# Optimization experiments

Measured on AMD Instinct MI355X. Metric: run time of the kernel, lower is better.

## Reference

```python
import jax, jax.numpy as jnp
import numpy as np

N = 100000   # total nodes (batched molecular graph)
E = 200000   # total edges
G = 5000     # number of graphs
NF = 16      # num_node_features
EF = 8       # num_edge_features
LD = 64      # latent_dim
EPS = 1e-5   # batch-norm eps (PyG BatchNorm default)


def setup_inputs() -> dict:
    key = jax.random.key(0)
    ks = jax.random.split(key, 20)
    s = 0.1  # weight scale
    return {
        'x': jax.random.normal(ks[0], (N, NF), dtype=jnp.float32),
        'edge_index': jax.random.randint(ks[1], (2, E), 0, N, dtype=jnp.int32),
        'edge_attr': jax.random.normal(ks[2], (E, EF), dtype=jnp.float32),
        'batch': jnp.sort(jax.random.randint(ks[3], (N,), 0, G, dtype=jnp.int32)),
        # ECC layer 1 (in=16 -> out=32)
        'We1': jax.random.normal(ks[4], (NF * 32, EF), dtype=jnp.float32) * s,
        'b1': jnp.zeros((32,), dtype=jnp.float32),
        'Wr1': jax.random.normal(ks[5], (32, NF), dtype=jnp.float32) * s,
        'g1': jnp.ones((32,), dtype=jnp.float32),
        'be1': jnp.zeros((32,), dtype=jnp.float32),
        # ECC layer 2 (in=32 -> out=64)
        'We2': jax.random.normal(ks[6], (32 * 64, EF), dtype=jnp.float32) * s,
        'b2': jnp.zeros((64,), dtype=jnp.float32),
        'Wr2': jax.random.normal(ks[7], (64, 32), dtype=jnp.float32) * s,
        'g2': jnp.ones((64,), dtype=jnp.float32),
        'be2': jnp.zeros((64,), dtype=jnp.float32),
        # dense tail
        'Wf1': jax.random.normal(ks[8], (128, 64), dtype=jnp.float32) * s,
        'bf1': jnp.zeros((128,), dtype=jnp.float32),
        'Wf2': jax.random.normal(ks[9], (2 * LD, 128), dtype=jnp.float32) * s,
        'bf2': jnp.zeros((2 * LD,), dtype=jnp.float32),
    }


def _ecc(x, src, dst, edge_attr, We, b, Wr, out_c):
    # theta: per-edge [out_c, in_c] filter matrices from edge features
    in_c = x.shape[1]
    theta = (edge_attr @ We.T).reshape(-1, out_c, in_c)       # [E, out, in]
    deg = jnp.zeros((x.shape[0],), x.dtype).at[src].add(1.0)   # degree over edge_index[0]
    norm = jnp.where(deg > 0, 1.0 / deg, 0.0)                  # [N]
    msg = jnp.einsum('eoi,ei->eo', theta, x[src]) * norm[src, None]  # [E, out]
    agg = jnp.zeros((x.shape[0], out_c), x.dtype).at[dst].add(msg)   # scatter-add
    return agg + b + x @ Wr.T


def _bn(x, g, be):
    # training-mode batch norm over the node dimension
    mu = jnp.mean(x, axis=0)
    var = jnp.mean((x - mu) ** 2, axis=0)
    return (x - mu) * jax.lax.rsqrt(var + EPS) * g + be


def reference(x, edge_index, edge_attr, batch,
              We1, b1, Wr1, g1, be1,
              We2, b2, Wr2, g2, be2,
              Wf1, bf1, Wf2, bf2):
    src, dst = edge_index[0], edge_index[1]
    h = _ecc(x, src, dst, edge_attr, We1, b1, Wr1, 32)
    h = jax.nn.relu(_bn(h, g1, be1))
    h = _ecc(h, src, dst, edge_attr, We2, b2, Wr2, 64)
    h = jax.nn.relu(_bn(h, g2, be2))
    # global mean pool over graphs
    sums = jax.ops.segment_sum(h, batch, num_segments=G)
    cnts = jax.ops.segment_sum(jnp.ones((h.shape[0],), h.dtype), batch, num_segments=G)
    pooled = sums / jnp.maximum(cnts, 1.0)[:, None]            # [G, 64]
    h = jax.nn.relu(pooled @ Wf1.T + bf1)
    out = h @ Wf2.T + bf2                                      # [G, 2*LD]
    mu_z = out[:, :LD]
    log_sigma = out[:, LD:]
    return mu_z, log_sigma
```

## Files before the change

### kernel.cpp

```cpp
#include <hip/hip_runtime.h>

#define NN 100000
#define NE 200000
#define NG 5000
#define EPSI 1e-5f
#define NBLK 98

using short8 = __attribute__((ext_vector_type(8))) short;
using f32x4  = __attribute__((ext_vector_type(4))) float;

static __device__ inline short bfbits(float f) {
    __bf16 b = (__bf16)f;
    return __builtin_bit_cast(short, b);
}
static __device__ inline float bf2f(short s) {
    unsigned u = ((unsigned)(unsigned short)s) << 16;
    return __builtin_bit_cast(float, u);
}

constexpr long FZ_NRM  = 0;
constexpr long FZ_STAT = NN;
constexpr long FZ_DCNT = NN + 512;
constexpr long ZN_FAST = 2L * NN + 512;
constexpr long O_OFFS  = ZN_FAST;
constexpr long O_CURS  = O_OFFS + NN;
constexpr long O_PERM  = O_CURS + NN;
constexpr long O_GLO   = O_PERM + NE;
constexpr long O_BSUM  = O_GLO + NG + 1;
constexpr long O_POOL  = O_BSUM + 256;
constexpr long O_H1    = O_POOL + 64L * NG;
constexpr long O_OUT2  = O_H1 + 32L * NN;
constexpr long O_MSG2  = O_OUT2 + 64L * NN;
constexpr long TOTAL_FAST = O_MSG2 + 64L * NE;

constexpr long B_NORM = 0;
constexpr long B_AGG1 = NN;
constexpr long B_AGG2 = B_AGG1 + 32L * NN;
constexpr long B_GSUM = B_AGG2 + 64L * NN;
constexpr long B_GCNT = B_GSUM + 64L * NG;
constexpr long B_STAT = B_GCNT + NG;
constexpr long ZERO_FB = B_STAT + 512;


__global__ void k_norm(float* __restrict__ deg) {
    int n = blockIdx.x * blockDim.x + threadIdx.x;
    if (n < NN) { float d = deg[n]; deg[n] = d > 0.f ? 1.f / d : 0.f; }
}

template <int CI, int COLS, bool BNIN>
__global__ void __launch_bounds__(64 * (COLS / 16))
k_edge_lds(const int* __restrict__ ei, const float* __restrict__ ea,
           const float* __restrict__ h, const float* __restrict__ W,
           const float* __restrict__ nrm,
           const float* __restrict__ scin, const float* __restrict__ shin,
           float* __restrict__ msg)
{
    constexpr int KS = CI / 4;
    constexpr int TILES = COLS / 16;
    constexpr int BT = 64 * TILES;
    constexpr int HP = (CI == 32) ? 36 : 20;
    constexpr int NGRP = NE / 16;
    constexpr int TPR = BT / 16;

    const int tid  = threadIdx.x;
    const int lane = tid & 63;
    const int wid  = tid >> 6;
    const int c = lane & 15;
    const int q = lane >> 4;

    short8 bfr[KS];
    {
        const float* wrow = W + (wid * 16 + c) * (CI * 8) + q * 8;
        #pragma unroll
        for (int kk = 0; kk < KS; ++kk) {
            const float* p = wrow + kk * 32;
            #pragma unroll
            for (int j = 0; j < 8; ++j) bfr[kk][j] = bfbits(p[j]);
        }
    }

    __shared__ float h_lds[2][16 * HP];
    __shared__ float ea_lds[2][16 * 9];

    const int hrow = tid / TPR;
    const int hj0  = (tid % TPR) * 2;
    const int erow = tid >> 3;
    const int ef   = tid & 7;
    const bool eact = (tid < 128);

    float bsc0 = 1.f, bsc1 = 1.f, bsh0 = 0.f, bsh1 = 0.f;
    if constexpr (BNIN) {
        bsc0 = scin[hj0]; bsc1 = scin[hj0 + 1];
        bsh0 = shin[hj0]; bsh1 = shin[hj0 + 1];
    }

    auto write = [&](int buf, float v0, float v1, float ev) {
        if constexpr (BNIN) {
            v0 = fmaxf(fmaf(v0, bsc0, bsh0), 0.f);
            v1 = fmaxf(fmaf(v1, bsc1, bsh1), 0.f);
        }
        h_lds[buf][hrow * HP + hj0]     = v0;
        h_lds[buf][hrow * HP + hj0 + 1] = v1;
        if (eact) ea_lds[buf][erow * 9 + ef] = ev;
    };

    auto compute = [&](int buf, long e0) {
        float ev[8];
        #pragma unroll
        for (int j = 0; j < 8; ++j) ev[j] = ea_lds[buf][c * 9 + j];
        f32x4 acc = {0.f, 0.f, 0.f, 0.f};
        #pragma unroll
        for (int kk = 0; kk < KS; ++kk) {
            float hv = h_lds[buf][c * HP + kk * 4 + q];
            short8 afr;
            #pragma unroll
            for (int j = 0; j < 8; ++j) afr[j] = bfbits(hv * ev[j]);
            acc = __builtin_amdgcn_mfma_f32_16x16x32_bf16(afr, bfr[kk], acc, 0, 0, 0);
        }
        #pragma unroll
        for (int t = 0; t < 4; ++t) {
            msg[(e0 + q * 4 + t) * COLS + wid * 16 + c] = acc[t];
        }
    };

    const int GD = gridDim.x;
    int g = blockIdx.x;
    if (g >= NGRP) return;

    int sh_c = ei[(long)g * 16 + hrow];
    int se_c = 0; if (eact) se_c = ei[(long)g * 16 + erow];
    int sh_n = 0, se_n = 0;
    {
        int gn0 = g + GD;
        if (gn0 < NGRP) {
            sh_n = ei[(long)gn0 * 16 + hrow];
            if (eact) se_n = ei[(long)gn0 * 16 + erow];
        }
    }
    float hv0, hv1, eav = 0.f;
    {
        const float* hp = h + (long)sh_c * CI + hj0;
        hv0 = hp[0]; hv1 = hp[1];
        if (eact) eav = ea[((long)g * 16 + erow) * 8 + ef] * nrm[se_c];
    }
    write(0, hv0, hv1, eav);
    __syncthreads();

    int p = 0;
    for (;;) {
        int gn = g + GD;
        bool more = (gn < NGRP);
        int gnn = gn + GD;
        int sh_f = 0, se_f = 0;
        if (gnn < NGRP) {
            sh_f = ei[(long)gnn * 16 + hrow];
            if (eact) se_f = ei[(long)gnn * 16 + erow];
        }
        if (more) {
            const float* hp = h + (long)sh_n * CI + hj0;
            hv0 = hp[0]; hv1 = hp[1];
            if (eact) eav = ea[((long)gn * 16 + erow) * 8 + ef] * nrm[se_n];
        }
        compute(p, (long)g * 16);
        if (!more) break;
        write(p ^ 1, hv0, hv1, eav);
        __syncthreads();
        sh_n = sh_f; se_n = se_f;
        g = gn; p ^= 1;
    }
}

template <int KS, int COLS>
__global__ void __launch_bounds__(256) k_edge_mfma_at(
    const int* __restrict__ ei, const float* __restrict__ ea,
    const float* __restrict__ h, const float* __restrict__ W,
    const float* __restrict__ nrm, float* __restrict__ outp)
{
    constexpr int TILES = COLS / 16;
    constexpr int CI = KS * 4;
    const int lane = threadIdx.x & 63;
    const int wid  = threadIdx.x >> 6;
    const int c = lane & 15;
    const int q = lane >> 4;
    const int gw = blockIdx.x * 4 + wid;
    const int ntile = gw % TILES;
    const int grp   = gw / TILES;
    if (grp >= NE / 16) return;
    short8 bfr[KS];
    {
        const float* wrow = W + (ntile * 16 + c) * (KS * 32) + q * 8;
        #pragma unroll
        for (int kk = 0; kk < KS; ++kk) {
            const float* p = wrow + kk * 32;
            #pragma unroll
            for (int j = 0; j < 8; ++j) bfr[kk][j] = bfbits(p[j]);
        }
    }
    const long e0 = (long)grp * 16;
    const long e  = e0 + c;
    const int  s  = ei[e];
    const float nv = nrm[s];
    float ev[8];
    {
        const float* p = ea + e * 8;
        #pragma unroll
        for (int j = 0; j < 8; ++j) ev[j] = p[j];
    }
    float hv[KS];
    {
        const float* hp = h + (long)s * CI + q;
        #pragma unroll
        for (int kk = 0; kk < KS; ++kk) hv[kk] = hp[kk * 4] * nv;
    }
    f32x4 acc = {0.f, 0.f, 0.f, 0.f};
    #pragma unroll
    for (int kk = 0; kk < KS; ++kk) {
        short8 afr;
        #pragma unroll
        for (int j = 0; j < 8; ++j) afr[j] = bfbits(hv[kk] * ev[j]);
        acc = __builtin_amdgcn_mfma_f32_16x16x32_bf16(afr, bfr[kk], acc, 0, 0, 0);
    }
    #pragma unroll
    for (int t = 0; t < 4; ++t) {
        int m = q * 4 + t;
        int d = ei[NE + e0 + m];
        atomicAdd(&outp[(long)d * COLS + ntile * 16 + c], acc[t]);
    }
}

template <int C>
__global__ void k_colstats(const float* __restrict__ v, float* __restrict__ sum,
                           float* __restrict__ ssq) {
    constexpr int RPB = 256 / C;
    const int c = threadIdx.x % C;
    const int r = threadIdx.x / C;
    float s = 0.f, q = 0.f;
    for (int n = blockIdx.x * RPB + r; n < NN; n += gridDim.x * RPB) {
        float val = v[(long)n * C + c];
        s += val; q += val * val;
    }
    __shared__ float ls[256], lq[256];
    ls[threadIdx.x] = s; lq[threadIdx.x] = q;
    __syncthreads();
    if (threadIdx.x < C) {
        float ts = 0.f, tq = 0.f;
        #pragma unroll
        for (int k = 0; k < RPB; ++k) { ts += ls[c + k * C]; tq += lq[c + k * C]; }
        atomicAdd(&sum[c], ts);
        atomicAdd(&ssq[c], tq);
    }
}

__global__ void k_fin(int C, const float* __restrict__ sum, const float* __restrict__ ssq,
                      const float* __restrict__ g, const float* __restrict__ be,
                      float* __restrict__ scale, float* __restrict__ shift) {
    int c = threadIdx.x;
    if (c < C) {
        float mu  = sum[c] / (float)NN;
        float var = ssq[c] / (float)NN - mu * mu;
        float rs  = rsqrtf(var + EPSI);
        float sc  = rs * g[c];
        scale[c] = sc;
        shift[c] = be[c] - mu * sc;
    }
}

__global__ void k_bnrelu32(const float* __restrict__ in, const float* __restrict__ scale,
                           const float* __restrict__ shift, float* __restrict__ outp) {
    long t = (long)blockIdx.x * blockDim.x + threadIdx.x;
    if (t < 32L * NN) {
        int c = (int)(t & 31);
        float v = in[t] * scale[c] + shift[c];
        outp[t] = v > 0.f ? v : 0.f;
    }
}

template <int CO>
__global__ void __launch_bounds__(256) k_msum(
    const float* __restrict__ msg, const int* __restrict__ offs,
    const int* __restrict__ dcnt, const int* __restrict__ perm,
    float* __restrict__ aggout)
{
    constexpr int CPN = CO / 4;
    long t = (long)blockIdx.x * 256 + threadIdx.x;
    long n = t / CPN;
    int chunk = (int)(t % CPN);
    if (n >= NN) return;
    int lo = offs[n], ct = dcnt[n];
    f32x4 a = {0.f, 0.f, 0.f, 0.f}, b = {0.f, 0.f, 0.f, 0.f};
    int j = 0;
    for (; j + 1 < ct; j += 2) {
        int ea0 = perm[lo + j];
        int ea1 = perm[lo + j + 1];
        a += *reinterpret_cast<const f32x4*>(msg + (long)ea0 * CO + chunk * 4);
        b += *reinterpret_cast<const f32x4*>(msg + (long)ea1 * CO + chunk * 4);
    }
    if (j < ct) {
        int ea0 = perm[lo + j];
        a += *reinterpret_cast<const f32x4*>(msg + (long)ea0 * CO + chunk * 4);
    }
    a += b;
    *reinterpret_cast<f32x4*>(aggout + n * CO + chunk * 4) = a;
}

template <int CI, int CO, bool BNIN>
__global__ void __launch_bounds__(256) k_root(
    const float* __restrict__ X, const float* __restrict__ W,
    const float* __restrict__ bias, const float* __restrict__ scin,
    const float* __restrict__ shin, float* __restrict__ Y,
    float* __restrict__ sum, float* __restrict__ ssq)
{
    constexpr int TILES = CO / 16;
    constexpr int MT = NN / 16;
    constexpr int MTPB = 4 / TILES;
    const int lane = threadIdx.x & 63;
    const int wid  = threadIdx.x >> 6;
    const int c = lane & 15;
    const int q = lane >> 4;
    const int ntile = (TILES == 4) ? wid : (wid & (TILES - 1));
    const int mtoff = (TILES == 4) ? 0 : (wid >> 1);
    const int o = ntile * 16 + c;
    const bool kvalid = (q * 8) < CI;

    short8 bhi = {0,0,0,0,0,0,0,0}, blo = {0,0,0,0,0,0,0,0};
    if (kvalid) {
        const float* wrow = W + (long)o * CI + q * 8;
        #pragma unroll
        for (int j = 0; j < 8; ++j) {
            float v = wrow[j];
            short h = bfbits(v);
            bhi[j] = h;
            blo[j] = bfbits(v - bf2f(h));
        }
    }
    float bsc[8], bsh[8];
    if constexpr (BNIN) {
        #pragma unroll
        for (int j = 0; j < 8; ++j) {
            bsc[j] = kvalid ? scin[q * 8 + j] : 0.f;
            bsh[j] = kvalid ? shin[q * 8 + j] : 0.f;
        }
    }
    const float bv = bias[o];
    float s_acc = 0.f, q_acc = 0.f;

    for (int mt = blockIdx.x * MTPB + mtoff; mt < MT; mt += gridDim.x * MTPB) {
        short8 ahi = {0,0,0,0,0,0,0,0}, alo = {0,0,0,0,0,0,0,0};
        if (kvalid) {
            const float* xp = X + (long)(mt * 16 + c) * CI + q * 8;
            #pragma unroll
            for (int j = 0; j < 8; ++j) {
                float v = xp[j];
                if constexpr (BNIN) v = fmaxf(fmaf(v, bsc[j], bsh[j]), 0.f);
                short h = bfbits(v);
                ahi[j] = h;
                alo[j] = bfbits(v - bf2f(h));
            }
        }
        f32x4 acc = {0.f, 0.f, 0.f, 0.f};
        acc = __builtin_amdgcn_mfma_f32_16x16x32_bf16(ahi, bhi, acc, 0, 0, 0);
        acc = __builtin_amdgcn_mfma_f32_16x16x32_bf16(ahi, blo, acc, 0, 0, 0);
        acc = __builtin_amdgcn_mfma_f32_16x16x32_bf16(alo, bhi, acc, 0, 0, 0);
        #pragma unroll
        for (int t4 = 0; t4 < 4; ++t4) {
            long r = (long)mt * 16 + q * 4 + t4;
            long idx = r * CO + o;
            float v = Y[idx] + acc[t4] + bv;
            Y[idx] = v;
            s_acc += v;
            q_acc = fmaf(v, v, q_acc);
        }
    }

    __shared__ float ls[256], lq[256];
    ls[threadIdx.x] = s_acc; lq[threadIdx.x] = q_acc;
    __syncthreads();
    if (threadIdx.x < CO) {
        int ch = threadIdx.x;
        int bw = ch >> 4;
        int cc = ch & 15;
        float ts = 0.f, tq = 0.f;
        if (TILES == 4) {
            #pragma unroll
            for (int q2 = 0; q2 < 4; ++q2) {
                ts += ls[bw * 64 + q2 * 16 + cc];
                tq += lq[bw * 64 + q2 * 16 + cc];
            }
        } else {
            #pragma unroll
            for (int w2 = 0; w2 < 2; ++w2) {
                int w = bw + w2 * 2;
                #pragma unroll
                for (int q2 = 0; q2 < 4; ++q2) {
                    ts += ls[w * 64 + q2 * 16 + cc];
                    tq += lq[w * 64 + q2 * 16 + cc];
                }
            }
        }
        atomicAdd(&sum[ch], ts);
        atomicAdd(&ssq[ch], tq);
    }
}

template <int K, int NO, bool RELU, bool SPLITOUT>
__global__ void __launch_bounds__(256) k_fcmm(
    const float* __restrict__ X, const float* __restrict__ W,
    const float* __restrict__ bias, float* __restrict__ Y)
{
    constexpr int KS = K / 32;
    constexpr int TILES = NO / 16;
    constexpr int MT = (NG + 15) / 16;
    const int lane = threadIdx.x & 63;
    const int wid  = threadIdx.x >> 6;
    const int c = lane & 15;
    const int q = lane >> 4;
    const int gw = blockIdx.x * 4 + wid;
    const int ntile = gw % TILES;
    const int mt    = gw / TILES;
    if (mt >= MT) return;

    short8 bhi[KS], blo[KS];
    {
        const float* wrow = W + (ntile * 16 + c) * K + q * 8;
        #pragma unroll
        for (int kk = 0; kk < KS; ++kk) {
            const float* p = wrow + kk * 32;
            #pragma unroll
            for (int j = 0; j < 8; ++j) {
                float v = p[j];
                short h = bfbits(v);
                bhi[kk][j] = h;
                blo[kk][j] = bfbits(v - bf2f(h));
            }
        }
    }

    int arow = mt * 16 + c;
    if (arow > NG - 1) arow = NG - 1;
    const float* xp = X + (long)arow * K + q * 8;

    f32x4 acc = {0.f, 0.f, 0.f, 0.f};
    #pragma unroll
    for (int kk = 0; kk < KS; ++kk) {
        const float* p = xp + kk * 32;
        short8 ahi, alo;
        #pragma unroll
        for (int j = 0; j < 8; ++j) {
            float v = p[j];
            short h = bfbits(v);
            ahi[j] = h;
            alo[j] = bfbits(v - bf2f(h));
        }
        acc = __builtin_amdgcn_mfma_f32_16x16x32_bf16(ahi, bhi[kk], acc, 0, 0, 0);
        acc = __builtin_amdgcn_mfma_f32_16x16x32_bf16(ahi, blo[kk], acc, 0, 0, 0);
        acc = __builtin_amdgcn_mfma_f32_16x16x32_bf16(alo, bhi[kk], acc, 0, 0, 0);
    }

    const int o = ntile * 16 + c;
    const float bv = bias[o];
    #pragma unroll
    for (int t = 0; t < 4; ++t) {
        int r = mt * 16 + q * 4 + t;
        if (r < NG) {
            float v = acc[t] + bv;
            if (RELU) v = v > 0.f ? v : 0.f;
            if (SPLITOUT) {
                if (o < 64) Y[(long)r * 64 + o] = v;
                else        Y[(long)NG * 64 + (long)r * 64 + (o - 64)] = v;
            } else {
                Y[(long)r * NO + o] = v;
            }
        }
    }
}

__global__ void k_fc(const float* __restrict__ pooled,
                     const float* __restrict__ Wf1, const float* __restrict__ bf1,
                     const float* __restrict__ Wf2, const float* __restrict__ bf2,
                     float* __restrict__ outp) {
    const int lane = threadIdx.x & 63;
    int gw = (blockIdx.x * blockDim.x + threadIdx.x) >> 6;
    int nw = (gridDim.x * blockDim.x) >> 6;
    for (int g = gw; g < NG; g += nw) {
        float pl = pooled[(long)g * 64 + lane];
        float f1a = bf1[lane], f1b = bf1[lane + 64];
        const float* w1a = Wf1 + lane * 64;
        const float* w1b = Wf1 + (lane + 64) * 64;
        #pragma unroll 8
        for (int i = 0; i < 64; ++i) {
            float pv = __shfl(pl, i);
            f1a += pv * w1a[i];
            f1b += pv * w1b[i];
        }
        f1a = f1a > 0.f ? f1a : 0.f;
        f1b = f1b > 0.f ? f1b : 0.f;
        float oa = bf2[lane], ob = bf2[lane + 64];
        const float* w2a = Wf2 + lane * 128;
        const float* w2b = Wf2 + (lane + 64) * 128;
        #pragma unroll 8
        for (int i = 0; i < 64; ++i) {
            float va = __shfl(f1a, i);
            float vb = __shfl(f1b, i);
            oa += va * w2a[i] + vb * w2a[64 + i];
            ob += va * w2b[i] + vb * w2b[64 + i];
        }
        outp[(long)g * 64 + lane] = oa;
        outp[(long)NG * 64 + (long)g * 64 + lane] = ob;
    }
}


__global__ void k_degcnt(const int* __restrict__ ei, float* __restrict__ deg,
                         int* __restrict__ dcnt) {
    int e = blockIdx.x * blockDim.x + threadIdx.x;
    if (e < NE) {
        atomicAdd(&deg[ei[e]], 1.0f);
        atomicAdd(&dcnt[ei[NE + e]], 1);
    }
}

__global__ void k_scanA(const int* __restrict__ dcnt, int* __restrict__ offs,
                        int* __restrict__ bsum, float* __restrict__ deg) {
    int tid = threadIdx.x, b = blockIdx.x;
    int base = b * 1024 + tid * 4;
    int v[4]; int t = 0;
    #pragma unroll
    for (int k = 0; k < 4; ++k) { v[k] = (base + k < NN) ? dcnt[base + k] : 0; t += v[k]; }
    #pragma unroll
    for (int k = 0; k < 4; ++k) {
        int i = base + k;
        if (i < NN) { float d = deg[i]; deg[i] = d > 0.f ? 1.f / d : 0.f; }
    }
    __shared__ int s[256];
    s[tid] = t;
    __syncthreads();
    for (int d = 1; d < 256; d <<= 1) {
        int x = (tid >= d) ? s[tid - d] : 0;
        __syncthreads();
        s[tid] += x;
        __syncthreads();
    }
    int excl = s[tid] - t;
    int o = excl;
    #pragma unroll
    for (int k = 0; k < 4; ++k) {
        if (base + k < NN) offs[base + k] = o;
        o += v[k];
    }
    if (tid == 255) bsum[b] = s[255];
}

__global__ void k_scanB(int* __restrict__ bsum) {
    int tid = threadIdx.x;
    __shared__ int s[128];
    int val = (tid < NBLK) ? bsum[tid] : 0;
    s[tid] = val;
    __syncthreads();
    for (int d = 1; d < 128; d <<= 1) {
        int x = (tid >= d) ? s[tid - d] : 0;
        __syncthreads();
        s[tid] += x;
        __syncthreads();
    }
    bsum[tid] = s[tid] - val;
}

__global__ void k_scanC(int* __restrict__ offs, int* __restrict__ curs,
                        const int* __restrict__ bsum) {
    int tid = threadIdx.x, b = blockIdx.x;
    int base = b * 1024 + tid * 4;
    int add = bsum[b];
    #pragma unroll
    for (int k = 0; k < 4; ++k) {
        int i = base + k;
        if (i < NN) { int o = offs[i] + add; offs[i] = o; curs[i] = o; }
    }
}

__global__ void k_scatter(const int* __restrict__ ei, int* __restrict__ curs,
                          int* __restrict__ perm, const int* __restrict__ batch,
                          int* __restrict__ glo) {
    int e = blockIdx.x * blockDim.x + threadIdx.x;
    if (e < NE) {
        int d = ei[NE + e];
        int pos = atomicAdd(&curs[d], 1);
        perm[pos] = e;
    }
    if (e <= NG) {
        int lo = 0, hi = NN;
        while (lo < hi) { int m = (lo + hi) >> 1; if (batch[m] < e) lo = m + 1; else hi = m; }
        glo[e] = lo;
    }
}

__global__ void k_poolg(const float* __restrict__ out2, const int* __restrict__ glo,
                        const float* __restrict__ scale, const float* __restrict__ shift,
                        float* __restrict__ pooled) {
    const int lane = threadIdx.x & 63;
    int g = (blockIdx.x * blockDim.x + threadIdx.x) >> 6;
    if (g >= NG) return;
    int lo = glo[g], hi = glo[g + 1];
    float sc = scale[lane], sh = shift[lane];
    float acc = 0.f;
    for (int n = lo; n < hi; ++n) {
        float v = out2[(long)n * 64 + lane] * sc + sh;
        acc += v > 0.f ? v : 0.f;
    }
    float m = (float)(hi - lo);
    pooled[(long)g * 64 + lane] = acc / (m > 1.f ? m : 1.f);
}


__global__ void k_deg(const int* __restrict__ ei, float* __restrict__ deg) {
    int e = blockIdx.x * blockDim.x + threadIdx.x;
    if (e < NE) atomicAdd(&deg[ei[e]], 1.0f);
}

template <int CI, int CO>
__global__ void k_nodeadd(const float* __restrict__ xin, const float* __restrict__ Wr,
                          const float* __restrict__ b, float* __restrict__ outp) {
    constexpr int NPW = 64 / CO;
    const int lane = threadIdx.x & 63;
    const int c = lane % CO;
    const int sub = lane / CO;
    float w[CI];
    #pragma unroll
    for (int i = 0; i < CI; ++i) w[i] = Wr[c * CI + i];
    float bias = b[c];
    int gw = (blockIdx.x * blockDim.x + threadIdx.x) >> 6;
    int nw = (gridDim.x * blockDim.x) >> 6;
    for (int n0 = gw * NPW; n0 < NN; n0 += nw * NPW) {
        int n = n0 + sub;
        if (n < NN) {
            const float* xp = xin + (long)n * CI;
            float acc = outp[(long)n * CO + c] + bias;
            #pragma unroll
            for (int i = 0; i < CI; ++i) acc += xp[i] * w[i];
            outp[(long)n * CO + c] = acc;
        }
    }
}

__global__ void k_pool_at(const float* __restrict__ out2, const int* __restrict__ batch,
                          const float* __restrict__ scale, const float* __restrict__ shift,
                          float* __restrict__ gsum) {
    long t = (long)blockIdx.x * blockDim.x + threadIdx.x;
    int c = (int)(t & 63);
    long n0 = (t >> 6) * 4;
    if (n0 >= NN) return;
    float sc = scale[c], sh = shift[c];
    float acc = 0.f;
    int gprev = batch[n0];
    #pragma unroll
    for (int k = 0; k < 4; ++k) {
        long n = n0 + k;
        if (n >= NN) break;
        int g = batch[n];
        float v = out2[n * 64 + c] * sc + sh;
        v = v > 0.f ? v : 0.f;
        if (g != gprev) {
            atomicAdd(&gsum[(long)gprev * 64 + c], acc);
            acc = 0.f; gprev = g;
        }
        acc += v;
    }
    atomicAdd(&gsum[(long)gprev * 64 + c], acc);
}

__global__ void k_cnt(const int* __restrict__ batch, float* __restrict__ gcnt) {
    int n = blockIdx.x * blockDim.x + threadIdx.x;
    if (n < NN) atomicAdd(&gcnt[batch[n]], 1.0f);
}

__global__ void k_div(float* __restrict__ gsum, const float* __restrict__ gcnt) {
    long t = (long)blockIdx.x * blockDim.x + threadIdx.x;
    if (t < 64L * NG) {
        float cnt = gcnt[t >> 6];
        gsum[t] = gsum[t] / (cnt > 1.f ? cnt : 1.f);
    }
}


extern "C" void kernel_launch(void* const* d_in, const int* in_sizes, int n_in,
                              void* d_out, int out_size, void* d_ws, size_t ws_size,
                              hipStream_t stream) {
    const float* x   = (const float*)d_in[0];
    const int*   ei  = (const int*)d_in[1];
    const float* ea  = (const float*)d_in[2];
    const int*   bat = (const int*)d_in[3];
    const float* We1 = (const float*)d_in[4];
    const float* b1  = (const float*)d_in[5];
    const float* Wr1 = (const float*)d_in[6];
    const float* g1  = (const float*)d_in[7];
    const float* be1 = (const float*)d_in[8];
    const float* We2 = (const float*)d_in[9];
    const float* b2  = (const float*)d_in[10];
    const float* Wr2 = (const float*)d_in[11];
    const float* g2  = (const float*)d_in[12];
    const float* be2 = (const float*)d_in[13];
    const float* Wf1 = (const float*)d_in[14];
    const float* bf1 = (const float*)d_in[15];
    const float* Wf2 = (const float*)d_in[16];
    const float* bf2 = (const float*)d_in[17];
    float* out = (float*)d_out;
    float* ws  = (float*)d_ws;
    int*   wsi = (int*)d_ws;

    if (ws_size >= (size_t)TOTAL_FAST * sizeof(float)) {
        float* nrm    = ws + FZ_NRM;
        float* st     = ws + FZ_STAT;
        int*   dcnt   = wsi + FZ_DCNT;
        int*   offs   = wsi + O_OFFS;
        int*   curs   = wsi + O_CURS;
        int*   perm   = wsi + O_PERM;
        int*   glo    = wsi + O_GLO;
        int*   bsum   = wsi + O_BSUM;
        float* pooled = ws + O_POOL;
        float* h1     = ws + O_H1;
        float* out2   = ws + O_OUT2;
        float* msg1   = ws + O_OUT2;
        float* msg2   = ws + O_MSG2;
        float* fc1out = ws + O_MSG2;
        float* sums1 = st;        float* ssq1 = st + 32;
        float* sums2 = st + 64;   float* ssq2 = st + 128;
        float* sc1   = st + 192;  float* sh1  = st + 224;
        float* sc2   = st + 256;  float* sh2  = st + 320;

        hipMemsetAsync(d_ws, 0, (size_t)ZN_FAST * sizeof(float), stream);

        k_degcnt<<<(NE + 255) / 256, 256, 0, stream>>>(ei, nrm, dcnt);
        k_scanA<<<NBLK, 256, 0, stream>>>(dcnt, offs, bsum, nrm);
        k_scanB<<<1, 128, 0, stream>>>(bsum);
        k_scanC<<<NBLK, 256, 0, stream>>>(offs, curs, bsum);
        k_scatter<<<(NE + 255) / 256, 256, 0, stream>>>(ei, curs, perm, bat, glo);

        k_edge_lds<16, 32, false><<<2048, 128, 0, stream>>>(
            ei, ea, x, We1, nrm, nullptr, nullptr, msg1);
        k_msum<32><<<3125, 256, 0, stream>>>(msg1, offs, dcnt, perm, h1);
        k_root<16, 32, false><<<512, 256, 0, stream>>>(
            x, Wr1, b1, nullptr, nullptr, h1, sums1, ssq1);
        k_fin<<<1, 64, 0, stream>>>(32, sums1, ssq1, g1, be1, sc1, sh1);

        k_edge_lds<32, 64, true><<<2048, 256, 0, stream>>>(
            ei, ea, h1, We2, nrm, sc1, sh1, msg2);
        k_msum<64><<<6250, 256, 0, stream>>>(msg2, offs, dcnt, perm, out2);
        k_root<32, 64, true><<<512, 256, 0, stream>>>(
            h1, Wr2, b2, sc1, sh1, out2, sums2, ssq2);
        k_fin<<<1, 64, 0, stream>>>(64, sums2, ssq2, g2, be2, sc2, sh2);

        k_poolg<<<1250, 256, 0, stream>>>(out2, glo, sc2, sh2, pooled);

        {
            constexpr int MT = (NG + 15) / 16;
            k_fcmm<64, 128, true,  false><<<(MT * 8 + 3) / 4, 256, 0, stream>>>(pooled, Wf1, bf1, fc1out);
            k_fcmm<128, 128, false, true><<<(MT * 8 + 3) / 4, 256, 0, stream>>>(fc1out, Wf2, bf2, out);
        }
    } else {
        float* nrm   = ws + B_NORM;
        float* agg1  = ws + B_AGG1;
        float* agg2  = ws + B_AGG2;
        float* gsum  = ws + B_GSUM;
        float* gcnt  = ws + B_GCNT;
        float* st    = ws + B_STAT;
        float* sums1 = st;        float* ssq1 = st + 32;
        float* sums2 = st + 64;   float* ssq2 = st + 128;
        float* sc1   = st + 192;  float* sh1  = st + 224;
        float* sc2   = st + 256;  float* sh2  = st + 320;

        hipMemsetAsync(d_ws, 0, (size_t)ZERO_FB * sizeof(float), stream);

        k_deg<<<(NE + 255) / 256, 256, 0, stream>>>(ei, nrm);
        k_norm<<<(NN + 255) / 256, 256, 0, stream>>>(nrm);

        k_edge_mfma_at<4, 32><<<6250, 256, 0, stream>>>(ei, ea, x, We1, nrm, agg1);
        k_nodeadd<16, 32><<<1024, 256, 0, stream>>>(x, Wr1, b1, agg1);
        k_colstats<32><<<1024, 256, 0, stream>>>(agg1, sums1, ssq1);
        k_fin<<<1, 64, 0, stream>>>(32, sums1, ssq1, g1, be1, sc1, sh1);
        k_bnrelu32<<<(int)((32L * NN + 255) / 256), 256, 0, stream>>>(agg1, sc1, sh1, agg1);

        k_edge_mfma_at<8, 64><<<12500, 256, 0, stream>>>(ei, ea, agg1, We2, nrm, agg2);
        k_nodeadd<32, 64><<<1024, 256, 0, stream>>>(agg1, Wr2, b2, agg2);
        k_colstats<64><<<1024, 256, 0, stream>>>(agg2, sums2, ssq2);
        k_fin<<<1, 64, 0, stream>>>(64, sums2, ssq2, g2, be2, sc2, sh2);

        k_pool_at<<<6250, 256, 0, stream>>>(agg2, bat, sc2, sh2, gsum);
        k_cnt<<<(NN + 255) / 256, 256, 0, stream>>>(bat, gcnt);
        k_div<<<(int)((64L * NG + 255) / 256), 256, 0, stream>>>(gsum, gcnt);
        k_fc<<<1250, 256, 0, stream>>>(gsum, Wf1, bf1, Wf2, bf2, out);
    }
}
```

Baseline: 200.9 us.

## Store edge messages in bf16 and process 32 edges per block iteration

Per-edge messages are now written as bf16 instead of fp32, which halves the traffic of the message write and of the gather in the segment-sum kernel; k_msum converts back to fp32 before accumulating. The LDS-staged edge kernel now handles 32 edges per group using float4 loads of node features, so all threads take part in loading edge attributes. It also pads the pool offset to a 4-aligned boundary. The cost is extra rounding error in the messages and more LDS and register use per block.

After: 191.7 us. -4.6%, faster.

```diff
diff --git a/kernel.cpp b/kernel.cpp
--- a/kernel.cpp
+++ b/kernel.cpp
@@ -27,7 +27,7 @@
 constexpr long O_PERM  = O_CURS + NN;
 constexpr long O_GLO   = O_PERM + NE;
 constexpr long O_BSUM  = O_GLO + NG + 1;
-constexpr long O_POOL  = O_BSUM + 256;
+constexpr long O_POOL  = ((O_BSUM + 256 + 3) & ~3L);
 constexpr long O_H1    = O_POOL + 64L * NG;
 constexpr long O_OUT2  = O_H1 + 32L * NN;
 constexpr long O_MSG2  = O_OUT2 + 64L * NN;
@@ -53,14 +53,15 @@
            const float* __restrict__ h, const float* __restrict__ W,
            const float* __restrict__ nrm,
            const float* __restrict__ scin, const float* __restrict__ shin,
-           float* __restrict__ msg)
+           unsigned short* __restrict__ msg)
 {
     constexpr int KS = CI / 4;
     constexpr int TILES = COLS / 16;
     constexpr int BT = 64 * TILES;
     constexpr int HP = (CI == 32) ? 36 : 20;
-    constexpr int NGRP = NE / 16;
-    constexpr int TPR = BT / 16;
+    constexpr int NGRP = NE / 32;
+    constexpr int TPR = BT / 32;
+    constexpr int EPT = 256 / BT;
 
     const int tid  = threadIdx.x;
     const int lane = tid & 63;
@@ -79,47 +80,56 @@
         }
     }
 
-    __shared__ float h_lds[2][16 * HP];
-    __shared__ float ea_lds[2][16 * 9];
+    __shared__ __align__(16) float h_lds[2][32 * HP];
+    __shared__ float ea_lds[2][32 * 9];
 
     const int hrow = tid / TPR;
-    const int hj0  = (tid % TPR) * 2;
+    const int hj0  = (tid % TPR) * 4;
     const int erow = tid >> 3;
     const int ef   = tid & 7;
-    const bool eact = (tid < 128);
-
-    float bsc0 = 1.f, bsc1 = 1.f, bsh0 = 0.f, bsh1 = 0.f;
+
+    float bsc0 = 1.f, bsc1 = 1.f, bsc2 = 1.f, bsc3 = 1.f;
+    float bsh0 = 0.f, bsh1 = 0.f, bsh2 = 0.f, bsh3 = 0.f;
     if constexpr (BNIN) {
-        bsc0 = scin[hj0]; bsc1 = scin[hj0 + 1];
-        bsh0 = shin[hj0]; bsh1 = shin[hj0 + 1];
-    }
-
-    auto write = [&](int buf, float v0, float v1, float ev) {
+        bsc0 = scin[hj0];     bsh0 = shin[hj0];
+        bsc1 = scin[hj0 + 1]; bsh1 = shin[hj0 + 1];
+        bsc2 = scin[hj0 + 2]; bsh2 = shin[hj0 + 2];
+        bsc3 = scin[hj0 + 3]; bsh3 = shin[hj0 + 3];
+    }
+
+    auto writebuf = [&](int buf, float4 hv, float ev0, float ev1) {
         if constexpr (BNIN) {
-            v0 = fmaxf(fmaf(v0, bsc0, bsh0), 0.f);
-            v1 = fmaxf(fmaf(v1, bsc1, bsh1), 0.f);
-        }
-        h_lds[buf][hrow * HP + hj0]     = v0;
-        h_lds[buf][hrow * HP + hj0 + 1] = v1;
-        if (eact) ea_lds[buf][erow * 9 + ef] = ev;
+            hv.x = fmaxf(fmaf(hv.x, bsc0, bsh0), 0.f);
+            hv.y = fmaxf(fmaf(hv.y, bsc1, bsh1), 0.f);
+            hv.z = fmaxf(fmaf(hv.z, bsc2, bsh2), 0.f);
+            hv.w = fmaxf(fmaf(hv.w, bsc3, bsh3), 0.f);
+        }
+        *reinterpret_cast<float4*>(&h_lds[buf][hrow * HP + hj0]) = hv;
+        ea_lds[buf][erow * 9 + ef] = ev0;
+        if constexpr (EPT == 2) ea_lds[buf][(erow + 16) * 9 + ef] = ev1;
     };
 
     auto compute = [&](int buf, long e0) {
-        float ev[8];
-        #pragma unroll
-        for (int j = 0; j < 8; ++j) ev[j] = ea_lds[buf][c * 9 + j];
-        f32x4 acc = {0.f, 0.f, 0.f, 0.f};
-        #pragma unroll
-        for (int kk = 0; kk < KS; ++kk) {
-            float hv = h_lds[buf][c * HP + kk * 4 + q];
-            short8 afr;
-            #pragma unroll
-            for (int j = 0; j < 8; ++j) afr[j] = bfbits(hv * ev[j]);
-            acc = __builtin_amdgcn_mfma_f32_16x16x32_bf16(afr, bfr[kk], acc, 0, 0, 0);
-        }
-        #pragma unroll
-        for (int t = 0; t < 4; ++t) {
-            msg[(e0 + q * 4 + t) * COLS + wid * 16 + c] = acc[t];
+        #pragma unroll
+        for (int et = 0; et < 2; ++et) {
+            const int r = et * 16 + c;
+            float ev[8];
+            #pragma unroll
+            for (int j = 0; j < 8; ++j) ev[j] = ea_lds[buf][r * 9 + j];
+            f32x4 acc = {0.f, 0.f, 0.f, 0.f};
+            #pragma unroll
+            for (int kk = 0; kk < KS; ++kk) {
+                float hv = h_lds[buf][r * HP + kk * 4 + q];
+                short8 afr;
+                #pragma unroll
+                for (int j = 0; j < 8; ++j) afr[j] = bfbits(hv * ev[j]);
+                acc = __builtin_amdgcn_mfma_f32_16x16x32_bf16(afr, bfr[kk], acc, 0, 0, 0);
+            }
+            #pragma unroll
+            for (int t = 0; t < 4; ++t) {
+                msg[(e0 + et * 16 + q * 4 + t) * COLS + wid * 16 + c] =
+                    (unsigned short)bfbits(acc[t]);
+            }
         }
     };
 
@@ -127,23 +137,28 @@
     int g = blockIdx.x;
     if (g >= NGRP) return;
 
-    int sh_c = ei[(long)g * 16 + hrow];
-    int se_c = 0; if (eact) se_c = ei[(long)g * 16 + erow];
-    int sh_n = 0, se_n = 0;
+    int sh_c = ei[(long)g * 32 + hrow];
+    int se0_c = ei[(long)g * 32 + erow];
+    int se1_c = 0;
+    if constexpr (EPT == 2) se1_c = ei[(long)g * 32 + erow + 16];
+    int sh_n = 0, se0_n = 0, se1_n = 0;
     {
         int gn0 = g + GD;
         if (gn0 < NGRP) {
-            sh_n = ei[(long)gn0 * 16 + hrow];
-            if (eact) se_n = ei[(long)gn0 * 16 + erow];
-        }
-    }
-    float hv0, hv1, eav = 0.f;
+            sh_n = ei[(long)gn0 * 32 + hrow];
+            se0_n = ei[(long)gn0 * 32 + erow];
+            if constexpr (EPT == 2) se1_n = ei[(long)gn0 * 32 + erow + 16];
+        }
+    }
+    float4 hv4;
+    float ev0 = 0.f, ev1 = 0.f;
     {
-        const float* hp = h + (long)sh_c * CI + hj0;
-        hv0 = hp[0]; hv1 = hp[1];
-        if (eact) eav = ea[((long)g * 16 + erow) * 8 + ef] * nrm[se_c];
-    }
-    write(0, hv0, hv1, eav);
+        hv4 = *reinterpret_cast<const float4*>(h + (long)sh_c * CI + hj0);
+        ev0 = ea[((long)g * 32 + erow) * 8 + ef] * nrm[se0_c];
+        if constexpr (EPT == 2)
+            ev1 = ea[((long)g * 32 + erow + 16) * 8 + ef] * nrm[se1_c];
+    }
+    writebuf(0, hv4, ev0, ev1);
     __syncthreads();
 
     int p = 0;
@@ -151,21 +166,23 @@
         int gn = g + GD;
         bool more = (gn < NGRP);
         int gnn = gn + GD;
-        int sh_f = 0, se_f = 0;
+        int sh_f = 0, se0_f = 0, se1_f = 0;
         if (gnn < NGRP) {
-            sh_f = ei[(long)gnn * 16 + hrow];
-            if (eact) se_f = ei[(long)gnn * 16 + erow];
+            sh_f = ei[(long)gnn * 32 + hrow];
+            se0_f = ei[(long)gnn * 32 + erow];
+            if constexpr (EPT == 2) se1_f = ei[(long)gnn * 32 + erow + 16];
         }
         if (more) {
-            const float* hp = h + (long)sh_n * CI + hj0;
-            hv0 = hp[0]; hv1 = hp[1];
-            if (eact) eav = ea[((long)gn * 16 + erow) * 8 + ef] * nrm[se_n];
-        }
-        compute(p, (long)g * 16);
+            hv4 = *reinterpret_cast<const float4*>(h + (long)sh_n * CI + hj0);
+            ev0 = ea[((long)gn * 32 + erow) * 8 + ef] * nrm[se0_n];
+            if constexpr (EPT == 2)
+                ev1 = ea[((long)gn * 32 + erow + 16) * 8 + ef] * nrm[se1_n];
+        }
+        compute(p, (long)g * 32);
         if (!more) break;
-        write(p ^ 1, hv0, hv1, eav);
+        writebuf(p ^ 1, hv4, ev0, ev1);
         __syncthreads();
-        sh_n = sh_f; se_n = se_f;
+        sh_n = sh_f; se0_n = se0_f; se1_n = se1_f;
         g = gn; p ^= 1;
     }
 }
@@ -277,7 +294,7 @@
 
 template <int CO>
 __global__ void __launch_bounds__(256) k_msum(
-    const float* __restrict__ msg, const int* __restrict__ offs,
+    const unsigned short* __restrict__ msg, const int* __restrict__ offs,
     const int* __restrict__ dcnt, const int* __restrict__ perm,
     float* __restrict__ aggout)
 {
@@ -290,14 +307,20 @@
     f32x4 a = {0.f, 0.f, 0.f, 0.f}, b = {0.f, 0.f, 0.f, 0.f};
     int j = 0;
     for (; j + 1 < ct; j += 2) {
-        int ea0 = perm[lo + j];
-        int ea1 = perm[lo + j + 1];
-        a += *reinterpret_cast<const f32x4*>(msg + (long)ea0 * CO + chunk * 4);
-        b += *reinterpret_cast<const f32x4*>(msg + (long)ea1 * CO + chunk * 4);
+        int e0p = perm[lo + j];
+        int e1p = perm[lo + j + 1];
+        ushort4 u0 = *reinterpret_cast<const ushort4*>(msg + (long)e0p * CO + chunk * 4);
+        ushort4 u1 = *reinterpret_cast<const ushort4*>(msg + (long)e1p * CO + chunk * 4);
+        a.x += bf2f((short)u0.x); a.y += bf2f((short)u0.y);
+        a.z += bf2f((short)u0.z); a.w += bf2f((short)u0.w);
+        b.x += bf2f((short)u1.x); b.y += bf2f((short)u1.y);
+        b.z += bf2f((short)u1.z); b.w += bf2f((short)u1.w);
     }
     if (j < ct) {
-        int ea0 = perm[lo + j];
-        a += *reinterpret_cast<const f32x4*>(msg + (long)ea0 * CO + chunk * 4);
+        int e0p = perm[lo + j];
+        ushort4 u0 = *reinterpret_cast<const ushort4*>(msg + (long)e0p * CO + chunk * 4);
+        a.x += bf2f((short)u0.x); a.y += bf2f((short)u0.y);
+        a.z += bf2f((short)u0.z); a.w += bf2f((short)u0.w);
     }
     a += b;
     *reinterpret_cast<f32x4*>(aggout + n * CO + chunk * 4) = a;
@@ -718,8 +741,8 @@
         float* pooled = ws + O_POOL;
         float* h1     = ws + O_H1;
         float* out2   = ws + O_OUT2;
-        float* msg1   = ws + O_OUT2;
-        float* msg2   = ws + O_MSG2;
+        unsigned short* msg1 = (unsigned short*)(ws + O_OUT2);
+        unsigned short* msg2 = (unsigned short*)(ws + O_MSG2);
         float* fc1out = ws + O_MSG2;
         float* sums1 = st;        float* ssq1 = st + 32;
         float* sums2 = st + 64;   float* ssq2 = st + 128;
```
